# Kernel tuning notes

Hardware: AMD Instinct MI355X
Metric: run time of the kernel (lower is better)

Reference implementation:

```python
import jax, jax.numpy as jnp
import numpy as np
from jax import lax

DIM = 256
RATE = 4
MAX_SK_IT = 10
N = RATE
NC = N * DIM            # 1024
NG = N * N + 2 * N      # 24


def setup_inputs() -> dict:
    key = jax.random.key(0)
    ks = jax.random.split(key, 5)
    h = jax.random.normal(ks[0], (8, 4096, N, DIM), jnp.float32)
    norm_weight = jax.random.normal(ks[1], (NC,), jnp.float32)
    w = jax.random.normal(ks[2], (NC, NG), jnp.float32) * 0.02
    alpha = jax.random.normal(ks[3], (3,), jnp.float32) * 0.01
    beta = jax.random.normal(ks[4], (NG,), jnp.float32) * 0.1
    return {"h": h, "norm_weight": norm_weight, "w": w, "alpha": alpha, "beta": beta}


def _sinkhorn(K, iters):
    # Sinkhorn-Knopp diagonal scalings u, v such that diag(u) @ K @ diag(v)
    # is (approximately) doubly stochastic. K: (BL, N, N) positive.
    BL, n, _ = K.shape
    u = jnp.ones((BL, n), K.dtype)
    v = jnp.ones((BL, n), K.dtype)

    def body(carry, _):
        u, v = carry
        u = 1.0 / (jnp.einsum('bij,bj->bi', K, v) + 1e-8)
        v = 1.0 / (jnp.einsum('bij,bi->bj', K, u) + 1e-8)
        return (u, v), None

    (u, v), _ = lax.scan(body, (u, v), None, length=iters)
    return u, v


def reference(h, norm_weight, w, alpha, beta):
    B, L, n, D = h.shape
    hf = h.reshape(B, L, n * D)              # (B,L,NC)
    hv = norm_weight * hf                    # mapping uses raw norm weight
    H = hv @ w                               # (B,L,NG)
    r = jnp.linalg.norm(hf, axis=-1, keepdims=True) / np.float32(np.sqrt(n * D))
    r_ = 1.0 / (r + 1e-6)

    H_pre = jax.nn.sigmoid(r_ * H[..., :n] * alpha[0] + beta[:n])            # (B,L,N)
    H_post = 2.0 * jax.nn.sigmoid(r_ * H[..., n:2 * n] * alpha[1] + beta[n:2 * n])
    H_res = (r_ * H[..., 2 * n:] * alpha[2] + beta[2 * n:]).reshape(B, L, n, n)

    K = jnp.exp(H_res).reshape(B * L, n, n)
    u, v = _sinkhorn(K, MAX_SK_IT)
    u = lax.stop_gradient(u)
    v = lax.stop_gradient(v)
    P = (u[:, :, None] * K * v[:, None, :]).reshape(B, L, n, n)

    # process
    h_pre = jnp.einsum('bln,blnd->bld', H_pre, h)[:, :, None, :]  # (B,L,1,D)
    h_res = jnp.einsum('blnm,blmd->blnd', P, h)                   # (B,L,N,D)

    # depth_connection with h_out = h_pre (identity inner layer)
    out = H_post[..., None] * h_pre + h_res                       # (B,L,N,D)
    return out
```

## Files before the change

kernel.cpp:

```cpp
#include <hip/hip_runtime.h>
#include <math.h>


#define NTOK 16

typedef __attribute__((ext_vector_type(2))) _Float16 h2v;

__device__ __forceinline__ float fdot2f(unsigned int a, unsigned int b, float c) {
#if __has_builtin(__builtin_amdgcn_fdot2)
    return __builtin_amdgcn_fdot2(__builtin_bit_cast(h2v, a),
                                  __builtin_bit_cast(h2v, b), c, false);
#else
    h2v av = __builtin_bit_cast(h2v, a);
    h2v bv = __builtin_bit_cast(h2v, b);
    return fmaf((float)av[1], (float)bv[1],
           fmaf((float)av[0], (float)bv[0], c));
#endif
}

__device__ __forceinline__ unsigned int pk_f16(float a, float b) {
    const auto p = __builtin_amdgcn_cvt_pkrtz(a, b);
    return __builtin_bit_cast(unsigned int, p);
}

__device__ __forceinline__ float sigmoid_f(float z) {
    return 1.0f / (1.0f + __expf(-z));
}

__device__ __forceinline__ float row16_sum(float x) {
    x += __int_as_float(__builtin_amdgcn_update_dpp(
        0, __float_as_int(x), 0x121, 0xf, 0xf, false));
    x += __int_as_float(__builtin_amdgcn_update_dpp(
        0, __float_as_int(x), 0x122, 0xf, 0xf, false));
    x += __int_as_float(__builtin_amdgcn_update_dpp(
        0, __float_as_int(x), 0x124, 0xf, 0xf, false));
    x += __int_as_float(__builtin_amdgcn_update_dpp(
        0, __float_as_int(x), 0x128, 0xf, 0xf, false));
    return x;
}

__global__ __launch_bounds__(256)
void prep_kernel(const float* __restrict__ nw,
                 const float* __restrict__ w,
                 const float* __restrict__ alpha,
                 unsigned short* __restrict__ wt)
{
    const int tid = blockIdx.x * 256 + threadIdx.x;
    const int flat = 4 * tid;
    const float4 w4 = *(const float4*)(w + flat);
    const float a0 = alpha[0], a1 = alpha[1], a2 = alpha[2];
    const float vals[4] = {w4.x, w4.y, w4.z, w4.w};
    #pragma unroll
    for (int c = 0; c < 4; ++c) {
        const int f = flat + c;
        const int k = f / 24;
        const int n = f - 24 * k;
        const float as = (n < 4) ? a0 : ((n < 8) ? a1 : a2);
        const unsigned int p = pk_f16(as * nw[k] * vals[c], 0.f);
        wt[n * 1024 + k] = (unsigned short)(p & 0xffffu);
    }
}

__global__ __launch_bounds__(256, 3)
void mhc_kernel(const float* __restrict__ h,
                const unsigned short* __restrict__ wt,
                const float* __restrict__ beta,
                float* __restrict__ out)
{
    const int tid  = threadIdx.x;
    const int lane = tid & 63;
    const int wv   = tid >> 6;
    const int ksl  = lane & 15;
    const int ng   = lane >> 4;

    __shared__ unsigned int tile[NTOK * 512];
    __shared__ float Hpart[NTOK][28];
    __shared__ float smalls[NTOK][26];

    const long tok0 = (long)blockIdx.x * NTOK;

    {
        const float* src = h + tok0 * 1024 + 4 * tid;
        #pragma unroll
        for (int i = 0; i < NTOK; ++i) {
            const float4 v = *(const float4*)(src + 1024 * i);
            uint2 u;
            u.x = pk_f16(v.x, v.y);
            u.y = pk_f16(v.z, v.w);
            *(uint2*)(tile + i * 512 + 2 * tid) = u;
        }
    }
    __syncthreads();

    const int t0 = 4 * wv;
    const uint2* txp = (const uint2*)tile + t0 * 256 + ksl;
    const uint2* twp = (const uint2*)wt + (6 * ng) * 256 + ksl;

    float acc[4][6], r2[4];
    #pragma unroll
    for (int t = 0; t < 4; ++t) {
        r2[t] = 0.f;
        #pragma unroll
        for (int j = 0; j < 6; ++j) acc[t][j] = 0.f;
    }

    #pragma unroll 1
    for (int e = 0; e < 16; ++e) {
        uint2 xw[4];
        #pragma unroll
        for (int t = 0; t < 4; ++t) xw[t] = txp[t * 256 + e * 16];
        uint2 wr[6];
        #pragma unroll
        for (int j = 0; j < 6; ++j) wr[j] = twp[j * 256 + e * 16];

        #pragma unroll
        for (int j = 0; j < 6; ++j) {
            #pragma unroll
            for (int t = 0; t < 4; ++t) {
                acc[t][j] = fdot2f(xw[t].y, wr[j].y,
                            fdot2f(xw[t].x, wr[j].x, acc[t][j]));
            }
        }
        #pragma unroll
        for (int t = 0; t < 4; ++t) {
            r2[t] = fdot2f(xw[t].y, xw[t].y,
                    fdot2f(xw[t].x, xw[t].x, r2[t]));
        }
    }

    #pragma unroll
    for (int t = 0; t < 4; ++t) {
        #pragma unroll
        for (int j = 0; j < 6; ++j) acc[t][j] = row16_sum(acc[t][j]);
        r2[t] = row16_sum(r2[t]);
    }
    if (ksl == 0) {
        #pragma unroll
        for (int t = 0; t < 4; ++t) {
            #pragma unroll
            for (int j = 0; j < 6; ++j)
                Hpart[t0 + t][6 * ng + j] = acc[t][j];
            if (ng == 0) Hpart[t0 + t][24] = r2[t];
        }
    }
    __syncthreads();

    if (tid < NTOK) {
        const int t = tid;
        float Hp[24];
        #pragma unroll
        for (int q = 0; q < 24; ++q) Hp[q] = Hpart[t][q];
        const float r2v = Hpart[t][24];
        const float r_ = 1.0f / (sqrtf(r2v) * 0.03125f + 1e-6f);

        float Hpre[4], Hpost[4], K[16];
        #pragma unroll
        for (int n = 0; n < 4; ++n)
            Hpre[n] = sigmoid_f(fmaf(r_, Hp[n], beta[n]));
        #pragma unroll
        for (int n = 0; n < 4; ++n)
            Hpost[n] = 2.0f * sigmoid_f(fmaf(r_, Hp[4 + n], beta[4 + n]));
        #pragma unroll
        for (int q = 0; q < 16; ++q)
            K[q] = __expf(fmaf(r_, Hp[8 + q], beta[8 + q]));

        float u0=1.f,u1=1.f,u2=1.f,u3=1.f;
        float v0=1.f,v1=1.f,v2=1.f,v3=1.f;
        for (int itr = 0; itr < 10; ++itr) {
            u0 = 1.0f/(K[0]*v0  + K[1]*v1  + K[2]*v2  + K[3]*v3  + 1e-8f);
            u1 = 1.0f/(K[4]*v0  + K[5]*v1  + K[6]*v2  + K[7]*v3  + 1e-8f);
            u2 = 1.0f/(K[8]*v0  + K[9]*v1  + K[10]*v2 + K[11]*v3 + 1e-8f);
            u3 = 1.0f/(K[12]*v0 + K[13]*v1 + K[14]*v2 + K[15]*v3 + 1e-8f);
            v0 = 1.0f/(K[0]*u0  + K[4]*u1  + K[8]*u2  + K[12]*u3 + 1e-8f);
            v1 = 1.0f/(K[1]*u0  + K[5]*u1  + K[9]*u2  + K[13]*u3 + 1e-8f);
            v2 = 1.0f/(K[2]*u0  + K[6]*u1  + K[10]*u2 + K[14]*u3 + 1e-8f);
            v3 = 1.0f/(K[3]*u0  + K[7]*u1  + K[11]*u2 + K[15]*u3 + 1e-8f);
        }
        smalls[t][0] = Hpre[0];  smalls[t][1] = Hpre[1];
        smalls[t][2] = Hpre[2];  smalls[t][3] = Hpre[3];
        smalls[t][4] = Hpost[0]; smalls[t][5] = Hpost[1];
        smalls[t][6] = Hpost[2]; smalls[t][7] = Hpost[3];
        smalls[t][8]  = u0*K[0]*v0;   smalls[t][9]  = u0*K[1]*v1;
        smalls[t][10] = u0*K[2]*v2;   smalls[t][11] = u0*K[3]*v3;
        smalls[t][12] = u1*K[4]*v0;   smalls[t][13] = u1*K[5]*v1;
        smalls[t][14] = u1*K[6]*v2;   smalls[t][15] = u1*K[7]*v3;
        smalls[t][16] = u2*K[8]*v0;   smalls[t][17] = u2*K[9]*v1;
        smalls[t][18] = u2*K[10]*v2;  smalls[t][19] = u2*K[11]*v3;
        smalls[t][20] = u3*K[12]*v0;  smalls[t][21] = u3*K[13]*v1;
        smalls[t][22] = u3*K[14]*v2;  smalls[t][23] = u3*K[15]*v3;
    }
    __syncthreads();

    const int gg = wv;
    for (int it = 0; it < NTOK; ++it) {
        const uint2* tl = (const uint2*)tile + it * 256 + lane;
        float xm[4][4];
        #pragma unroll
        for (int m = 0; m < 4; ++m) {
            const uint2 u = tl[m * 64];
            const h2v p0 = __builtin_bit_cast(h2v, u.x);
            const h2v p1 = __builtin_bit_cast(h2v, u.y);
            xm[m][0] = (float)p0[0]; xm[m][1] = (float)p0[1];
            xm[m][2] = (float)p1[0]; xm[m][3] = (float)p1[1];
        }

        const float hp0 = smalls[it][0], hp1 = smalls[it][1];
        const float hp2 = smalls[it][2], hp3 = smalls[it][3];
        const float hpost = smalls[it][4 + gg];
        const float P0 = smalls[it][8 + 4*gg + 0];
        const float P1 = smalls[it][8 + 4*gg + 1];
        const float P2 = smalls[it][8 + 4*gg + 2];
        const float P3 = smalls[it][8 + 4*gg + 3];

        float4 o;
        #pragma unroll
        for (int c = 0; c < 4; ++c) {
            const float hpre = hp0*xm[0][c] + hp1*xm[1][c]
                             + hp2*xm[2][c] + hp3*xm[3][c];
            const float res  = P0*xm[0][c] + P1*xm[1][c]
                             + P2*xm[2][c] + P3*xm[3][c];
            ((float*)&o)[c] = fmaf(hpost, hpre, res);
        }
        *(float4*)(out + (tok0 + it) * 1024 + gg * 256 + 4 * lane) = o;
    }
}

extern "C" void kernel_launch(void* const* d_in, const int* in_sizes, int n_in,
                              void* d_out, int out_size, void* d_ws, size_t ws_size,
                              hipStream_t stream) {
    const float* h     = (const float*)d_in[0];
    const float* nw    = (const float*)d_in[1];
    const float* w     = (const float*)d_in[2];
    const float* alpha = (const float*)d_in[3];
    const float* beta  = (const float*)d_in[4];
    float* out = (float*)d_out;
    unsigned short* wt = (unsigned short*)d_ws;

    prep_kernel<<<24, 256, 0, stream>>>(nw, w, alpha, wt);
    mhc_kernel<<<2048, 256, 0, stream>>>(h, wt, beta, out);
}
```

Measured before the change: 76.02 us.

## Drop fp16 LDS tile; read h from global in both phases with prefetch

Removes the shared-memory fp16 staging tile and its barrier. The GEMV phase now loads h directly from global memory and converts it to fp16 in registers, while the norm is computed in fp32. The output phase re-reads h from global in full fp32 with a two-token register prefetch, which also removes the fp16 rounding from the output. This lowers LDS use and drops the occupancy hint, at the cost of reading h twice from global (second read hopefully served by L2/MALL) and more registers.

```diff
diff --git a/kernel.cpp b/kernel.cpp
--- a/kernel.cpp
+++ b/kernel.cpp
@@ -61,7 +61,7 @@
     }
 }
 
-__global__ __launch_bounds__(256, 3)
+__global__ __launch_bounds__(256)
 void mhc_kernel(const float* __restrict__ h,
                 const unsigned short* __restrict__ wt,
                 const float* __restrict__ beta,
@@ -73,27 +73,12 @@
     const int ksl  = lane & 15;
     const int ng   = lane >> 4;
 
-    __shared__ unsigned int tile[NTOK * 512];
     __shared__ float Hpart[NTOK][28];
     __shared__ float smalls[NTOK][26];
 
     const long tok0 = (long)blockIdx.x * NTOK;
-
-    {
-        const float* src = h + tok0 * 1024 + 4 * tid;
-        #pragma unroll
-        for (int i = 0; i < NTOK; ++i) {
-            const float4 v = *(const float4*)(src + 1024 * i);
-            uint2 u;
-            u.x = pk_f16(v.x, v.y);
-            u.y = pk_f16(v.z, v.w);
-            *(uint2*)(tile + i * 512 + 2 * tid) = u;
-        }
-    }
-    __syncthreads();
-
     const int t0 = 4 * wv;
-    const uint2* txp = (const uint2*)tile + t0 * 256 + ksl;
+    const float* ph = h + (tok0 + t0) * 1024 + 4 * ksl;
     const uint2* twp = (const uint2*)wt + (6 * ng) * 256 + ksl;
 
     float acc[4][6], r2[4];
@@ -106,12 +91,20 @@
 
     #pragma unroll 1
     for (int e = 0; e < 16; ++e) {
+        float4 xf[4];
+        #pragma unroll
+        for (int t = 0; t < 4; ++t)
+            xf[t] = *(const float4*)(ph + t * 1024 + 64 * e);
+        uint2 wr[6];
+        #pragma unroll
+        for (int j = 0; j < 6; ++j) wr[j] = twp[j * 256 + e * 16];
+
         uint2 xw[4];
         #pragma unroll
-        for (int t = 0; t < 4; ++t) xw[t] = txp[t * 256 + e * 16];
-        uint2 wr[6];
-        #pragma unroll
-        for (int j = 0; j < 6; ++j) wr[j] = twp[j * 256 + e * 16];
+        for (int t = 0; t < 4; ++t) {
+            xw[t].x = pk_f16(xf[t].x, xf[t].y);
+            xw[t].y = pk_f16(xf[t].z, xf[t].w);
+        }
 
         #pragma unroll
         for (int j = 0; j < 6; ++j) {
@@ -123,8 +116,8 @@
         }
         #pragma unroll
         for (int t = 0; t < 4; ++t) {
-            r2[t] = fdot2f(xw[t].y, xw[t].y,
-                    fdot2f(xw[t].x, xw[t].x, r2[t]));
+            r2[t] = fmaf(xf[t].w, xf[t].w, fmaf(xf[t].z, xf[t].z,
+                    fmaf(xf[t].y, xf[t].y, fmaf(xf[t].x, xf[t].x, r2[t]))));
         }
     }
 
@@ -192,18 +185,24 @@
     __syncthreads();
 
     const int gg = wv;
+    const float* p0 = h + tok0 * 1024 + 4 * lane;
+    float4 ca0, ca1, ca2, ca3, cb0, cb1, cb2, cb3;
+    {
+        ca0 = *(const float4*)(p0);       ca1 = *(const float4*)(p0 + 256);
+        ca2 = *(const float4*)(p0 + 512); ca3 = *(const float4*)(p0 + 768);
+        const float* q = p0 + 1024;
+        cb0 = *(const float4*)(q);        cb1 = *(const float4*)(q + 256);
+        cb2 = *(const float4*)(q + 512);  cb3 = *(const float4*)(q + 768);
+    }
     for (int it = 0; it < NTOK; ++it) {
-        const uint2* tl = (const uint2*)tile + it * 256 + lane;
-        float xm[4][4];
-        #pragma unroll
-        for (int m = 0; m < 4; ++m) {
-            const uint2 u = tl[m * 64];
-            const h2v p0 = __builtin_bit_cast(h2v, u.x);
-            const h2v p1 = __builtin_bit_cast(h2v, u.y);
-            xm[m][0] = (float)p0[0]; xm[m][1] = (float)p0[1];
-            xm[m][2] = (float)p1[0]; xm[m][3] = (float)p1[1];
-        }
-
+        const long tok = tok0 + it;
+        const float4 xm0 = ca0, xm1 = ca1, xm2 = ca2, xm3 = ca3;
+        ca0 = cb0; ca1 = cb1; ca2 = cb2; ca3 = cb3;
+        if (it + 2 < NTOK) {
+            const float* p = p0 + (it + 2) * 1024;
+            cb0 = *(const float4*)(p);       cb1 = *(const float4*)(p + 256);
+            cb2 = *(const float4*)(p + 512); cb3 = *(const float4*)(p + 768);
+        }
         const float hp0 = smalls[it][0], hp1 = smalls[it][1];
         const float hp2 = smalls[it][2], hp3 = smalls[it][3];
         const float hpost = smalls[it][4 + gg];
@@ -213,15 +212,23 @@
         const float P3 = smalls[it][8 + 4*gg + 3];
 
         float4 o;
-        #pragma unroll
-        for (int c = 0; c < 4; ++c) {
-            const float hpre = hp0*xm[0][c] + hp1*xm[1][c]
-                             + hp2*xm[2][c] + hp3*xm[3][c];
-            const float res  = P0*xm[0][c] + P1*xm[1][c]
-                             + P2*xm[2][c] + P3*xm[3][c];
-            ((float*)&o)[c] = fmaf(hpost, hpre, res);
-        }
-        *(float4*)(out + (tok0 + it) * 1024 + gg * 256 + 4 * lane) = o;
+        {
+            const float hpre = hp0*xm0.x + hp1*xm1.x + hp2*xm2.x + hp3*xm3.x;
+            o.x = fmaf(hpost, hpre, P0*xm0.x + P1*xm1.x + P2*xm2.x + P3*xm3.x);
+        }
+        {
+            const float hpre = hp0*xm0.y + hp1*xm1.y + hp2*xm2.y + hp3*xm3.y;
+            o.y = fmaf(hpost, hpre, P0*xm0.y + P1*xm1.y + P2*xm2.y + P3*xm3.y);
+        }
+        {
+            const float hpre = hp0*xm0.z + hp1*xm1.z + hp2*xm2.z + hp3*xm3.z;
+            o.z = fmaf(hpost, hpre, P0*xm0.z + P1*xm1.z + P2*xm2.z + P3*xm3.z);
+        }
+        {
+            const float hpre = hp0*xm0.w + hp1*xm1.w + hp2*xm2.w + hp3*xm3.w;
+            o.w = fmaf(hpost, hpre, P0*xm0.w + P1*xm1.w + P2*xm2.w + P3*xm3.w);
+        }
+        *(float4*)(out + tok * 1024 + gg * 256 + 4 * lane) = o;
     }
 }
 
```

Result: slower. 82.48 us (+8.5%).

## Make each wave own its four tokens end-to-end and drop block barriers

Applied to the files above, without the earlier changes.

Each wave now loads, converts, projects, runs Sinkhorn on and writes out its own four tokens, so the block-wide __syncthreads are replaced by per-wave LDS waitcnt fences. The epilogue computes the h_pre mix once per token and reuses it across all four output streams, instead of each wave recomputing it for its own stream. The launch_bounds occupancy hint is removed. Waves no longer stall on each other, but only 4 lanes per wave run the serial Sinkhorn step, and register pressure may rise without the occupancy hint.

```diff
diff --git a/kernel.cpp b/kernel.cpp
--- a/kernel.cpp
+++ b/kernel.cpp
@@ -25,6 +25,11 @@
 
 __device__ __forceinline__ float sigmoid_f(float z) {
     return 1.0f / (1.0f + __expf(-z));
+}
+
+__device__ __forceinline__ void wave_lds_fence() {
+    asm volatile("s_waitcnt lgkmcnt(0)" ::: "memory");
+    __builtin_amdgcn_sched_barrier(0);
 }
 
 __device__ __forceinline__ float row16_sum(float x) {
@@ -61,7 +66,7 @@
     }
 }
 
-__global__ __launch_bounds__(256, 3)
+__global__ __launch_bounds__(256)
 void mhc_kernel(const float* __restrict__ h,
                 const unsigned short* __restrict__ wt,
                 const float* __restrict__ beta,
@@ -78,21 +83,25 @@
     __shared__ float smalls[NTOK][26];
 
     const long tok0 = (long)blockIdx.x * NTOK;
+    const int t0 = 4 * wv;
 
     {
-        const float* src = h + tok0 * 1024 + 4 * tid;
-        #pragma unroll
-        for (int i = 0; i < NTOK; ++i) {
-            const float4 v = *(const float4*)(src + 1024 * i);
-            uint2 u;
-            u.x = pk_f16(v.x, v.y);
-            u.y = pk_f16(v.z, v.w);
-            *(uint2*)(tile + i * 512 + 2 * tid) = u;
-        }
-    }
-    __syncthreads();
-
-    const int t0 = 4 * wv;
+        #pragma unroll
+        for (int r = 0; r < 4; ++r) {
+            const float* src = h + (tok0 + t0 + r) * 1024 + 4 * lane;
+            unsigned int* dst = tile + (t0 + r) * 512;
+            #pragma unroll
+            for (int q = 0; q < 4; ++q) {
+                const float4 v = *(const float4*)(src + 256 * q);
+                uint2 u;
+                u.x = pk_f16(v.x, v.y);
+                u.y = pk_f16(v.z, v.w);
+                *(uint2*)(dst + 2 * (lane + 64 * q)) = u;
+            }
+        }
+    }
+    wave_lds_fence();
+
     const uint2* txp = (const uint2*)tile + t0 * 256 + ksl;
     const uint2* twp = (const uint2*)wt + (6 * ng) * 256 + ksl;
 
@@ -143,10 +152,10 @@
             if (ng == 0) Hpart[t0 + t][24] = r2[t];
         }
     }
-    __syncthreads();
-
-    if (tid < NTOK) {
-        const int t = tid;
+    wave_lds_fence();
+
+    if (lane < 4) {
+        const int t = t0 + lane;
         float Hp[24];
         #pragma unroll
         for (int q = 0; q < 24; ++q) Hp[q] = Hpart[t][q];
@@ -189,10 +198,11 @@
         smalls[t][20] = u3*K[12]*v0;  smalls[t][21] = u3*K[13]*v1;
         smalls[t][22] = u3*K[14]*v2;  smalls[t][23] = u3*K[15]*v3;
     }
-    __syncthreads();
-
-    const int gg = wv;
-    for (int it = 0; it < NTOK; ++it) {
+    wave_lds_fence();
+
+    #pragma unroll
+    for (int r = 0; r < 4; ++r) {
+        const int it = t0 + r;
         const uint2* tl = (const uint2*)tile + it * 256 + lane;
         float xm[4][4];
         #pragma unroll
@@ -206,22 +216,28 @@
 
         const float hp0 = smalls[it][0], hp1 = smalls[it][1];
         const float hp2 = smalls[it][2], hp3 = smalls[it][3];
-        const float hpost = smalls[it][4 + gg];
-        const float P0 = smalls[it][8 + 4*gg + 0];
-        const float P1 = smalls[it][8 + 4*gg + 1];
-        const float P2 = smalls[it][8 + 4*gg + 2];
-        const float P3 = smalls[it][8 + 4*gg + 3];
-
-        float4 o;
-        #pragma unroll
-        for (int c = 0; c < 4; ++c) {
-            const float hpre = hp0*xm[0][c] + hp1*xm[1][c]
-                             + hp2*xm[2][c] + hp3*xm[3][c];
-            const float res  = P0*xm[0][c] + P1*xm[1][c]
-                             + P2*xm[2][c] + P3*xm[3][c];
-            ((float*)&o)[c] = fmaf(hpost, hpre, res);
-        }
-        *(float4*)(out + (tok0 + it) * 1024 + gg * 256 + 4 * lane) = o;
+
+        float hpre[4];
+        #pragma unroll
+        for (int c = 0; c < 4; ++c)
+            hpre[c] = hp0*xm[0][c] + hp1*xm[1][c] + hp2*xm[2][c] + hp3*xm[3][c];
+
+        #pragma unroll
+        for (int n = 0; n < 4; ++n) {
+            const float hpost = smalls[it][4 + n];
+            const float P0 = smalls[it][8 + 4*n + 0];
+            const float P1 = smalls[it][8 + 4*n + 1];
+            const float P2 = smalls[it][8 + 4*n + 2];
+            const float P3 = smalls[it][8 + 4*n + 3];
+            float4 o;
+            #pragma unroll
+            for (int c = 0; c < 4; ++c) {
+                const float res = P0*xm[0][c] + P1*xm[1][c]
+                                + P2*xm[2][c] + P3*xm[3][c];
+                ((float*)&o)[c] = fmaf(hpost, hpre[c], res);
+            }
+            *(float4*)(out + (tok0 + it) * 1024 + n * 256 + 4 * lane) = o;
+        }
     }
 }
 
```

Result: no change. 76.93 us (+1.2%).
